# Optimization experiments

Hardware: AMD Instinct MI355X
Metric: run time of the kernel (lower is better)

Reference implementation:

```python
import jax, jax.numpy as jnp
import numpy as np
import math

HID = 128
NH = 8
HD = HID // NH
NL = 3
CLIP = 10.0
EPS = 1e-5

def _ln(x, g, b):
    mu = jnp.mean(x, axis=-1, keepdims=True)
    var = jnp.var(x, axis=-1, keepdims=True)
    return (x - mu) * jax.lax.rsqrt(var + EPS) * g + b

def _layer(h, e_bias1, e_gate2, g1, b1, wh, g2, b2, w1, w2):
    B, N, _ = h.shape
    h_in = h
    hn = _ln(h, g1, b1)
    qkv = hn @ wh                                   # (B,N,3H)
    q, k, v = jnp.split(qkv, 3, axis=-1)
    q = q.reshape(B, N, NH, HD).transpose(0, 2, 1, 3)  # (B,nh,N,hd)
    k = k.reshape(B, N, NH, HD).transpose(0, 2, 1, 3)
    v = v.reshape(B, N, NH, HD).transpose(0, 2, 1, 3)
    att = jnp.einsum('bhid,bhjd->bhij', q, k) * (1.0 / math.sqrt(HD))
    att = jax.nn.softmax(att + e_bias1, axis=-1) * e_gate2
    y = jnp.einsum('bhij,bhjd->bhid', att, v)
    y = y.transpose(0, 2, 1, 3).reshape(B, N, HID)
    z = _ln(y + h_in, g2, b2)
    mlp = jax.nn.relu(z @ w1) @ w2
    return mlp + y

def setup_inputs() -> dict:
    key = jax.random.key(0)
    ks = jax.random.split(key, 9)
    d = {
        'node_features': jax.random.normal(ks[0], (16, 256, 2), jnp.float32),
        'edge_features': jax.random.normal(ks[1], (16, 256, 256, 1), jnp.float32),
        'Wn': jax.random.normal(ks[2], (2, HID), jnp.float32) * 0.5,
        'We_in': jax.random.normal(ks[3], (1, HID), jnp.float32) * 0.1,
        'ln1_g': jnp.ones((NL, HID), jnp.float32),
        'ln1_b': jnp.zeros((NL, HID), jnp.float32),
        'Wh': jax.random.normal(ks[4], (NL, HID, 3 * HID), jnp.float32) * (1.0 / math.sqrt(HID)),
        'We': jax.random.normal(ks[5], (NL, HID, 2 * NH), jnp.float32) * (1.0 / math.sqrt(HID)),
        'ln2_g': jnp.ones((NL, HID), jnp.float32),
        'ln2_b': jnp.zeros((NL, HID), jnp.float32),
        'W1': jax.random.normal(ks[6], (NL, HID, 4 * HID), jnp.float32) * (1.0 / math.sqrt(HID)),
        'W2': jax.random.normal(ks[7], (NL, 4 * HID, HID), jnp.float32) * (1.0 / math.sqrt(4 * HID)),
        'Wdec': jax.random.normal(ks[8], (HID, 1), jnp.float32) * (1.0 / math.sqrt(HID)),
    }
    return d

def reference(node_features, edge_features, Wn, We_in, ln1_g, ln1_b, Wh, We, ln2_g, ln2_b, W1, W2, Wdec):
    h = node_features @ Wn                              # (B,N,H)
    e = edge_features @ We_in                           # (B,N,N,H)
    for i in range(NL):
        ee = e @ We[i]                                  # (B,N,N,2*nh)
        ee = ee.transpose(0, 3, 1, 2)                   # (B,2*nh,N,N)
        e1, e2 = ee[:, :NH], ee[:, NH:]
        h = _layer(h, e1, e2, ln1_g[i], ln1_b[i], Wh[i], ln2_g[i], ln2_b[i], W1[i], W2[i])
    out = h @ Wdec                                      # (B,N,1)
    out = CLIP * jnp.tanh(out / math.sqrt(HID))
    return out
```

## Files before the change

kernel.cpp:

```cpp
#include <hip/hip_runtime.h>
#include <math.h>

#define HID 128
#define NHEAD 8
#define NL 3
#define NS 256
#define ROWS 4096

typedef __attribute__((ext_vector_type(8))) short bf16x8;
typedef __attribute__((ext_vector_type(4))) float f32x4;

__device__ __forceinline__ float us2f(unsigned short s) { return __uint_as_float(((unsigned)s) << 16); }
__device__ __forceinline__ unsigned short f2b(float f) {
    unsigned u = __float_as_uint(f);
    return (unsigned short)((u + 0x7fff + ((u >> 16) & 1)) >> 16);
}

__global__ __launch_bounds__(256) void k_prep(
    const float* __restrict__ Wh, const float* __restrict__ W1, const float* __restrict__ W2,
    const float* __restrict__ We_in, const float* __restrict__ We,
    const float* __restrict__ nf, const float* __restrict__ Wn,
    unsigned short* __restrict__ WhH, unsigned short* __restrict__ WhL,
    unsigned short* __restrict__ W1H, unsigned short* __restrict__ W1L,
    unsigned short* __restrict__ W2H, unsigned short* __restrict__ W2L,
    float* __restrict__ sbuf, float* __restrict__ h)
{
    int b = blockIdx.x, t = threadIdx.x;
    if (b >= 529) {
        int idx = (b - 529) * 256 + t;
        int r = idx >> 7, c = idx & 127;
        h[idx] = nf[2 * r] * Wn[c] + nf[2 * r + 1] * Wn[HID + c];
        return;
    }
    if (b == 528) {
        if (t < NL * 2 * NHEAD) {
            int l = t / (2 * NHEAD), j = t % (2 * NHEAD);
            float acc = 0.f;
            for (int c = 0; c < HID; ++c)
                acc += We_in[c] * We[(long)(l * HID + c) * (2 * NHEAD) + j];
            sbuf[t] = acc;
        }
        return;
    }
    const float* S; unsigned short *OH, *OL; int K, N, kt, nt;
    if (b < 144) {
        int l = b / 48, rem = b % 48; kt = rem & 3; nt = rem >> 2; K = 128; N = 384;
        S = Wh + (long)l * 128 * 384; OH = WhH + (long)l * 384 * 128; OL = WhL + (long)l * 384 * 128;
    } else if (b < 336) {
        int b2 = b - 144; int l = b2 / 64, rem = b2 % 64; kt = rem & 3; nt = rem >> 2; K = 128; N = 512;
        S = W1 + (long)l * 128 * 512; OH = W1H + (long)l * 512 * 128; OL = W1L + (long)l * 512 * 128;
    } else {
        int b2 = b - 336; int l = b2 / 64, rem = b2 % 64; kt = rem & 15; nt = rem >> 4; K = 512; N = 128;
        S = W2 + (long)l * 512 * 128; OH = W2H + (long)l * 128 * 512; OL = W2L + (long)l * 128 * 512;
    }
    __shared__ float sm[32][33];
    int i0 = t >> 5, j = t & 31;
#pragma unroll
    for (int p = 0; p < 4; ++p) {
        int i = i0 + p * 8;
        sm[i][j] = S[(long)(kt * 32 + i) * N + nt * 32 + j];
    }
    __syncthreads();
#pragma unroll
    for (int p = 0; p < 4; ++p) {
        int n = i0 + p * 8;
        float v = sm[j][n];
        unsigned short hh = f2b(v);
        long o = (long)(nt * 32 + n) * K + kt * 32 + j;
        OH[o] = hh; OL[o] = f2b(v - us2f(hh));
    }
}

__global__ __launch_bounds__(256) void k_fgemm(
    const float* __restrict__ x, const float* __restrict__ x2,
    const float* __restrict__ g, const float* __restrict__ b,
    const unsigned short* __restrict__ WH, const unsigned short* __restrict__ WL,
    float* __restrict__ Cf, unsigned short* __restrict__ Ch, unsigned short* __restrict__ Cl,
    int Nc, int mode)
{
    __shared__ unsigned short sAh[64 * 136], sAl[64 * 136];
    __shared__ unsigned short sWh[64 * 136], sWl[64 * 136];
    int t = threadIdx.x;
    int row0 = blockIdx.y * 64, col0 = blockIdx.x * 64;

#pragma unroll
    for (int p = 0; p < 4; ++p) {
        int rr = (t >> 4) + p * 16, ck = t & 15;
        *(uint4*)&sWh[rr * 136 + ck * 8] = *(const uint4*)&WH[(long)(col0 + rr) * 128 + ck * 8];
        *(uint4*)&sWl[rr * 136 + ck * 8] = *(const uint4*)&WL[(long)(col0 + rr) * 128 + ck * 8];
    }
#pragma unroll
    for (int pass = 0; pass < 2; ++pass) {
        int row = pass * 32 + (t >> 3);
        int p = t & 7, cb = p * 16;
        float v[16];
        const float* xp = x + (long)(row0 + row) * HID + cb;
#pragma unroll
        for (int j = 0; j < 16; j += 4) *(float4*)&v[j] = *(const float4*)(xp + j);
        if (x2) {
            const float* yp = x2 + (long)(row0 + row) * HID + cb;
#pragma unroll
            for (int j = 0; j < 16; j += 4) {
                float4 r4 = *(const float4*)(yp + j);
                v[j] += r4.x; v[j+1] += r4.y; v[j+2] += r4.z; v[j+3] += r4.w;
            }
        }
        float s = 0.f, s2 = 0.f;
#pragma unroll
        for (int j = 0; j < 16; ++j) { s += v[j]; s2 += v[j] * v[j]; }
        s  += __shfl_xor(s, 1);  s  += __shfl_xor(s, 2);  s  += __shfl_xor(s, 4);
        s2 += __shfl_xor(s2, 1); s2 += __shfl_xor(s2, 2); s2 += __shfl_xor(s2, 4);
        float mu  = s * (1.f / HID);
        float var = s2 * (1.f / HID) - mu * mu;
        float inv = rsqrtf(var + 1e-5f);
        unsigned short hi[16], lo[16];
#pragma unroll
        for (int j = 0; j < 16; ++j) {
            int c = cb + j;
            float o = (v[j] - mu) * inv * g[c] + b[c];
            hi[j] = f2b(o); lo[j] = f2b(o - us2f(hi[j]));
        }
        *(uint4*)&sAh[row * 136 + cb]     = *(uint4*)&hi[0];
        *(uint4*)&sAh[row * 136 + cb + 8] = *(uint4*)&hi[8];
        *(uint4*)&sAl[row * 136 + cb]     = *(uint4*)&lo[0];
        *(uint4*)&sAl[row * 136 + cb + 8] = *(uint4*)&lo[8];
    }
    __syncthreads();

    int w = t >> 6, lane = t & 63;
    int m = lane & 15, quad = lane >> 4;
    f32x4 acc[4];
#pragma unroll
    for (int i = 0; i < 4; ++i) acc[i] = (f32x4){0.f, 0.f, 0.f, 0.f};
#pragma unroll
    for (int c = 0; c < 4; ++c) {
        bf16x8 ah = *(const bf16x8*)&sAh[(w * 16 + m) * 136 + c * 32 + quad * 8];
        bf16x8 al = *(const bf16x8*)&sAl[(w * 16 + m) * 136 + c * 32 + quad * 8];
#pragma unroll
        for (int nt = 0; nt < 4; ++nt) {
            bf16x8 wh = *(const bf16x8*)&sWh[(nt * 16 + m) * 136 + c * 32 + quad * 8];
            bf16x8 wl = *(const bf16x8*)&sWl[(nt * 16 + m) * 136 + c * 32 + quad * 8];
            acc[nt] = __builtin_amdgcn_mfma_f32_16x16x32_bf16(ah, wh, acc[nt], 0, 0, 0);
            acc[nt] = __builtin_amdgcn_mfma_f32_16x16x32_bf16(ah, wl, acc[nt], 0, 0, 0);
            acc[nt] = __builtin_amdgcn_mfma_f32_16x16x32_bf16(al, wh, acc[nt], 0, 0, 0);
        }
    }
#pragma unroll
    for (int nt = 0; nt < 4; ++nt) {
#pragma unroll
        for (int r = 0; r < 4; ++r) {
            int row = row0 + w * 16 + quad * 4 + r;
            int col = col0 + nt * 16 + m;
            float v = acc[nt][r];
            if (mode == 0) {
                Cf[(long)row * Nc + col] = v;
            } else {
                v = fmaxf(v, 0.f);
                unsigned short hh = f2b(v);
                Ch[(long)row * Nc + col] = hh;
                Cl[(long)row * Nc + col] = f2b(v - us2f(hh));
            }
        }
    }
}

__global__ __launch_bounds__(256, 3) void k_w2ln(
    const unsigned short* __restrict__ Ah, const unsigned short* __restrict__ Al,
    const unsigned short* __restrict__ WH, const unsigned short* __restrict__ WL,
    const float* __restrict__ yres, float* __restrict__ hout,
    const float* __restrict__ Wdec, float* __restrict__ out)
{
    __shared__ unsigned short sA[2][16 * 72];
    __shared__ unsigned short sW[2][128 * 72];
    int t = threadIdx.x;
    int row0 = blockIdx.x * 16;
    int w = t >> 6, lane = t & 63;
    int m = lane & 15, quad = lane >> 4;
    f32x4 acc[2];
    acc[0] = (f32x4){0.f,0.f,0.f,0.f}; acc[1] = (f32x4){0.f,0.f,0.f,0.f};

    for (int ks = 0; ks < 512; ks += 64) {
        if (ks) __syncthreads();
        {
            int pl = t >> 7, tt = t & 127;
            int r = tt >> 3, ck = tt & 7;
            const unsigned short* src = pl ? Al : Ah;
            *(uint4*)&sA[pl][r * 72 + ck * 8] = *(const uint4*)&src[(long)(row0 + r) * 512 + ks + ck * 8];
        }
        {
            int r0 = t >> 3, ck = t & 7;
#pragma unroll
            for (int p = 0; p < 4; ++p) {
                int n = r0 + p * 32;
                *(uint4*)&sW[0][n * 72 + ck * 8] = *(const uint4*)&WH[(long)n * 512 + ks + ck * 8];
                *(uint4*)&sW[1][n * 72 + ck * 8] = *(const uint4*)&WL[(long)n * 512 + ks + ck * 8];
            }
        }
        __syncthreads();
#pragma unroll
        for (int c = 0; c < 2; ++c) {
            bf16x8 ah = *(const bf16x8*)&sA[0][m * 72 + c * 32 + quad * 8];
            bf16x8 al = *(const bf16x8*)&sA[1][m * 72 + c * 32 + quad * 8];
#pragma unroll
            for (int nt = 0; nt < 2; ++nt) {
                int n = w * 32 + nt * 16 + m;
                bf16x8 wh = *(const bf16x8*)&sW[0][n * 72 + c * 32 + quad * 8];
                bf16x8 wl = *(const bf16x8*)&sW[1][n * 72 + c * 32 + quad * 8];
                acc[nt] = __builtin_amdgcn_mfma_f32_16x16x32_bf16(ah, wh, acc[nt], 0, 0, 0);
                acc[nt] = __builtin_amdgcn_mfma_f32_16x16x32_bf16(ah, wl, acc[nt], 0, 0, 0);
                acc[nt] = __builtin_amdgcn_mfma_f32_16x16x32_bf16(al, wh, acc[nt], 0, 0, 0);
            }
        }
    }
    __syncthreads();
    float* ht = (float*)&sW[0][0];
#pragma unroll
    for (int nt = 0; nt < 2; ++nt) {
#pragma unroll
        for (int r = 0; r < 4; ++r) {
            int row = quad * 4 + r;
            int col = w * 32 + nt * 16 + m;
            float v = acc[nt][r] + yres[(long)(row0 + row) * HID + col];
            hout[(long)(row0 + row) * HID + col] = v;
            ht[row * 132 + col] = v;
        }
    }
    __syncthreads();
    if (Wdec) {
        int row = t >> 4, sub = t & 15;
        float v[8];
        *(float4*)&v[0] = *(const float4*)&ht[row * 132 + sub * 8];
        *(float4*)&v[4] = *(const float4*)&ht[row * 132 + sub * 8 + 4];
        float a = 0.f;
#pragma unroll
        for (int j = 0; j < 8; ++j) a += v[j] * Wdec[sub * 8 + j];
        a += __shfl_xor(a, 1); a += __shfl_xor(a, 2); a += __shfl_xor(a, 4); a += __shfl_xor(a, 8);
        if (sub == 0) out[row0 + row] = 10.f * tanhf(a * 0.08838834764831845f);
    }
}

#define PAS (NS + 8)
__global__ __launch_bounds__(256) void k_attn(const float* __restrict__ qkv,
                                              const float* __restrict__ ef,
                                              const float* __restrict__ sbuf,
                                              int layer,
                                              float* __restrict__ y) {
    __shared__ float Ks[NS][20];
    __shared__ unsigned short Vh[16][PAS];
    __shared__ unsigned short Vl[16][PAS];
    __shared__ unsigned short Pa[4][16][PAS];
    int bid = blockIdx.x;
    int q4 = bid & 3, hh = (bid >> 2) & 7, bb = bid >> 5;
    int t = threadIdx.x;
    {
        const float* kr = qkv + ((long)(bb * NS + t)) * 384 + HID + hh * 16;
        *(float4*)&Ks[t][0]  = *(const float4*)kr;
        *(float4*)&Ks[t][4]  = *(const float4*)(kr + 4);
        *(float4*)&Ks[t][8]  = *(const float4*)(kr + 8);
        *(float4*)&Ks[t][12] = *(const float4*)(kr + 12);
        const float* vr = kr + HID;
        float vv[16];
        *(float4*)&vv[0]  = *(const float4*)vr;
        *(float4*)&vv[4]  = *(const float4*)(vr + 4);
        *(float4*)&vv[8]  = *(const float4*)(vr + 8);
        *(float4*)&vv[12] = *(const float4*)(vr + 12);
#pragma unroll
        for (int d = 0; d < 16; ++d) {
            unsigned short hi = f2b(vv[d]);
            Vh[d][t] = hi;
            Vl[d][t] = f2b(vv[d] - us2f(hi));
        }
    }
    __syncthreads();
    int w = t >> 6, lane = t & 63;
    float s1  = sbuf[layer * 16 + hh];
    float s2g = sbuf[layer * 16 + NHEAD + hh];
    int m = lane & 15, quad = lane >> 4;
    unsigned short* Paw = &Pa[w][0][0];
    for (int it = 0; it < 4; ++it) {
        int r0 = q4 * 64 + w * 16 + it * 4;
        float q[4][16];
#pragma unroll
        for (int rr = 0; rr < 4; ++rr) {
            const float* qr = qkv + ((long)(bb * NS + r0 + rr)) * 384 + hh * 16;
            *(float4*)&q[rr][0]  = *(const float4*)qr;
            *(float4*)&q[rr][4]  = *(const float4*)(qr + 4);
            *(float4*)&q[rr][8]  = *(const float4*)(qr + 8);
            *(float4*)&q[rr][12] = *(const float4*)(qr + 12);
        }
        float sc[4][4];
#pragma unroll
        for (int i = 0; i < 4; ++i) {
            int c = i * 64 + lane;
            float kk[16];
            *(float4*)&kk[0]  = *(const float4*)&Ks[c][0];
            *(float4*)&kk[4]  = *(const float4*)&Ks[c][4];
            *(float4*)&kk[8]  = *(const float4*)&Ks[c][8];
            *(float4*)&kk[12] = *(const float4*)&Ks[c][12];
#pragma unroll
            for (int rr = 0; rr < 4; ++rr) {
                float d0 = 0.f;
#pragma unroll
                for (int d = 0; d < 16; ++d) d0 += q[rr][d] * kk[d];
                sc[rr][i] = d0;
            }
        }
#pragma unroll
        for (int rr = 0; rr < 4; ++rr) {
            long eb = ((long)(bb * NS + r0 + rr)) * NS;
            float e0 = ef[eb + lane],       e1 = ef[eb + 64 + lane];
            float e2 = ef[eb + 128 + lane], e3 = ef[eb + 192 + lane];
            float x0 = sc[rr][0] * 0.25f + e0 * s1;
            float x1 = sc[rr][1] * 0.25f + e1 * s1;
            float x2 = sc[rr][2] * 0.25f + e2 * s1;
            float x3 = sc[rr][3] * 0.25f + e3 * s1;
            float mm = fmaxf(fmaxf(x0, x1), fmaxf(x2, x3));
#pragma unroll
            for (int o = 32; o; o >>= 1) mm = fmaxf(mm, __shfl_xor(mm, o));
            float p0 = __expf(x0 - mm), p1 = __expf(x1 - mm);
            float p2 = __expf(x2 - mm), p3 = __expf(x3 - mm);
            float sum = p0 + p1 + p2 + p3;
#pragma unroll
            for (int o = 32; o; o >>= 1) sum += __shfl_xor(sum, o);
            float inv = s2g / sum;
            int prow = it * 4 + rr;
            Paw[prow * PAS + lane]       = f2b(p0 * inv * e0);
            Paw[prow * PAS + 64 + lane]  = f2b(p1 * inv * e1);
            Paw[prow * PAS + 128 + lane] = f2b(p2 * inv * e2);
            Paw[prow * PAS + 192 + lane] = f2b(p3 * inv * e3);
        }
    }
    f32x4 acc = (f32x4){0.f, 0.f, 0.f, 0.f};
#pragma unroll
    for (int s = 0; s < 8; ++s) {
        bf16x8 pf = *(const bf16x8*)&Paw[m * PAS + s * 32 + quad * 8];
        bf16x8 vh = *(const bf16x8*)&Vh[m][s * 32 + quad * 8];
        bf16x8 vl = *(const bf16x8*)&Vl[m][s * 32 + quad * 8];
        acc = __builtin_amdgcn_mfma_f32_16x16x32_bf16(pf, vh, acc, 0, 0, 0);
        acc = __builtin_amdgcn_mfma_f32_16x16x32_bf16(pf, vl, acc, 0, 0, 0);
    }
#pragma unroll
    for (int r = 0; r < 4; ++r) {
        int row = q4 * 64 + w * 16 + quad * 4 + r;
        y[((long)(bb * NS + row)) * HID + hh * 16 + m] = acc[r];
    }
}

extern "C" void kernel_launch(void* const* d_in, const int* in_sizes, int n_in,
                              void* d_out, int out_size, void* d_ws, size_t ws_size,
                              hipStream_t stream) {
    const float* nf    = (const float*)d_in[0];
    const float* ef    = (const float*)d_in[1];
    const float* Wn    = (const float*)d_in[2];
    const float* We_in = (const float*)d_in[3];
    const float* ln1g  = (const float*)d_in[4];
    const float* ln1b  = (const float*)d_in[5];
    const float* Wh    = (const float*)d_in[6];
    const float* We    = (const float*)d_in[7];
    const float* ln2g  = (const float*)d_in[8];
    const float* ln2b  = (const float*)d_in[9];
    const float* W1    = (const float*)d_in[10];
    const float* W2    = (const float*)d_in[11];
    const float* Wdec  = (const float*)d_in[12];

    float* ws   = (float*)d_ws;
    float* sbuf = ws;
    float* h    = ws + 64;
    float* y    = h + ROWS * HID;
    float* qkv  = y + ROWS * HID;
    unsigned short* hidH = (unsigned short*)(qkv + (long)ROWS * 384);
    unsigned short* hidL = hidH + (long)ROWS * 512;
    unsigned short* WhH  = hidL + (long)ROWS * 512;
    unsigned short* WhL  = WhH + (long)NL * 384 * 128;
    unsigned short* W1H  = WhL + (long)NL * 384 * 128;
    unsigned short* W1L  = W1H + (long)NL * 512 * 128;
    unsigned short* W2H  = W1L + (long)NL * 512 * 128;
    unsigned short* W2L  = W2H + (long)NL * 128 * 512;

    k_prep<<<529 + ROWS * HID / 256, 256, 0, stream>>>(Wh, W1, W2, We_in, We, nf, Wn,
                                    WhH, WhL, W1H, W1L, W2H, W2L, sbuf, h);
    for (int l = 0; l < NL; ++l) {
        k_fgemm<<<dim3(6, 64), 256, 0, stream>>>(h, nullptr,
            ln1g + l * HID, ln1b + l * HID,
            WhH + (long)l * 384 * 128, WhL + (long)l * 384 * 128,
            qkv, nullptr, nullptr, 384, 0);
        k_attn<<<512, 256, 0, stream>>>(qkv, ef, sbuf, l, y);
        k_fgemm<<<dim3(8, 64), 256, 0, stream>>>(y, h,
            ln2g + l * HID, ln2b + l * HID,
            W1H + (long)l * 512 * 128, W1L + (long)l * 512 * 128,
            nullptr, hidH, hidL, 512, 1);
        int last = (l == NL - 1);
        k_w2ln<<<ROWS / 16, 256, 0, stream>>>(hidH, hidL,
            W2H + (long)l * 128 * 512, W2L + (long)l * 128 * 512,
            y, h, last ? Wdec : nullptr, (float*)d_out);
    }
}
```

Baseline: 231.6 us.

## Fuse input embedding into first GEMM, split W2 by columns, drop softmax max

The node embedding moves out of the prep kernel and into the first LN+QKV GEMM, which also writes h. The W2 GEMM is split into two 64-column tiles to double the block count, and the decoder becomes its own small kernel. In fgemm the weight loads are issued into registers before the LayerNorm work so their latency overlaps it. Attention softmax drops the max subtraction, which saves a reduction but risks exp overflow for large logits. A barrier is also added before the P·V MMA.

```diff
diff --git a/kernel.cpp b/kernel.cpp
--- a/kernel.cpp
+++ b/kernel.cpp
@@ -19,19 +19,12 @@
 __global__ __launch_bounds__(256) void k_prep(
     const float* __restrict__ Wh, const float* __restrict__ W1, const float* __restrict__ W2,
     const float* __restrict__ We_in, const float* __restrict__ We,
-    const float* __restrict__ nf, const float* __restrict__ Wn,
     unsigned short* __restrict__ WhH, unsigned short* __restrict__ WhL,
     unsigned short* __restrict__ W1H, unsigned short* __restrict__ W1L,
     unsigned short* __restrict__ W2H, unsigned short* __restrict__ W2L,
-    float* __restrict__ sbuf, float* __restrict__ h)
+    float* __restrict__ sbuf)
 {
     int b = blockIdx.x, t = threadIdx.x;
-    if (b >= 529) {
-        int idx = (b - 529) * 256 + t;
-        int r = idx >> 7, c = idx & 127;
-        h[idx] = nf[2 * r] * Wn[c] + nf[2 * r + 1] * Wn[HID + c];
-        return;
-    }
     if (b == 528) {
         if (t < NL * 2 * NHEAD) {
             int l = t / (2 * NHEAD), j = t % (2 * NHEAD);
@@ -73,6 +66,7 @@
 
 __global__ __launch_bounds__(256) void k_fgemm(
     const float* __restrict__ x, const float* __restrict__ x2,
+    const float* __restrict__ nf, const float* __restrict__ Wn, float* __restrict__ hout,
     const float* __restrict__ g, const float* __restrict__ b,
     const unsigned short* __restrict__ WH, const unsigned short* __restrict__ WL,
     float* __restrict__ Cf, unsigned short* __restrict__ Ch, unsigned short* __restrict__ Cl,
@@ -83,26 +77,40 @@
     int t = threadIdx.x;
     int row0 = blockIdx.y * 64, col0 = blockIdx.x * 64;
 
-#pragma unroll
-    for (int p = 0; p < 4; ++p) {
-        int rr = (t >> 4) + p * 16, ck = t & 15;
-        *(uint4*)&sWh[rr * 136 + ck * 8] = *(const uint4*)&WH[(long)(col0 + rr) * 128 + ck * 8];
-        *(uint4*)&sWl[rr * 136 + ck * 8] = *(const uint4*)&WL[(long)(col0 + rr) * 128 + ck * 8];
+    uint4 wreg[8];
+    {
+        int rr0 = t >> 4, ck = t & 15;
+#pragma unroll
+        for (int p = 0; p < 4; ++p) {
+            wreg[p]     = *(const uint4*)&WH[(long)(col0 + rr0 + p * 16) * 128 + ck * 8];
+            wreg[4 + p] = *(const uint4*)&WL[(long)(col0 + rr0 + p * 16) * 128 + ck * 8];
+        }
     }
 #pragma unroll
     for (int pass = 0; pass < 2; ++pass) {
         int row = pass * 32 + (t >> 3);
         int p = t & 7, cb = p * 16;
         float v[16];
-        const float* xp = x + (long)(row0 + row) * HID + cb;
-#pragma unroll
-        for (int j = 0; j < 16; j += 4) *(float4*)&v[j] = *(const float4*)(xp + j);
-        if (x2) {
-            const float* yp = x2 + (long)(row0 + row) * HID + cb;
-#pragma unroll
-            for (int j = 0; j < 16; j += 4) {
-                float4 r4 = *(const float4*)(yp + j);
-                v[j] += r4.x; v[j+1] += r4.y; v[j+2] += r4.z; v[j+3] += r4.w;
+        if (nf) {
+            float n0 = nf[2 * (row0 + row)], n1 = nf[2 * (row0 + row) + 1];
+#pragma unroll
+            for (int j = 0; j < 16; ++j) v[j] = n0 * Wn[cb + j] + n1 * Wn[HID + cb + j];
+            if (blockIdx.x == 0) {
+#pragma unroll
+                for (int j = 0; j < 16; j += 4)
+                    *(float4*)&hout[(long)(row0 + row) * HID + cb + j] = *(float4*)&v[j];
+            }
+        } else {
+            const float* xp = x + (long)(row0 + row) * HID + cb;
+#pragma unroll
+            for (int j = 0; j < 16; j += 4) *(float4*)&v[j] = *(const float4*)(xp + j);
+            if (x2) {
+                const float* yp = x2 + (long)(row0 + row) * HID + cb;
+#pragma unroll
+                for (int j = 0; j < 16; j += 4) {
+                    float4 r4 = *(const float4*)(yp + j);
+                    v[j] += r4.x; v[j+1] += r4.y; v[j+2] += r4.z; v[j+3] += r4.w;
+                }
             }
         }
         float s = 0.f, s2 = 0.f;
@@ -124,6 +132,14 @@
         *(uint4*)&sAh[row * 136 + cb + 8] = *(uint4*)&hi[8];
         *(uint4*)&sAl[row * 136 + cb]     = *(uint4*)&lo[0];
         *(uint4*)&sAl[row * 136 + cb + 8] = *(uint4*)&lo[8];
+    }
+    {
+        int rr0 = t >> 4, ck = t & 15;
+#pragma unroll
+        for (int p = 0; p < 4; ++p) {
+            *(uint4*)&sWh[(rr0 + p * 16) * 136 + ck * 8] = wreg[p];
+            *(uint4*)&sWl[(rr0 + p * 16) * 136 + ck * 8] = wreg[4 + p];
+        }
     }
     __syncthreads();
 
@@ -164,20 +180,18 @@
     }
 }
 
-__global__ __launch_bounds__(256, 3) void k_w2ln(
+__global__ __launch_bounds__(256, 4) void k_w2(
     const unsigned short* __restrict__ Ah, const unsigned short* __restrict__ Al,
     const unsigned short* __restrict__ WH, const unsigned short* __restrict__ WL,
-    const float* __restrict__ yres, float* __restrict__ hout,
-    const float* __restrict__ Wdec, float* __restrict__ out)
+    const float* __restrict__ yres, float* __restrict__ hout)
 {
     __shared__ unsigned short sA[2][16 * 72];
-    __shared__ unsigned short sW[2][128 * 72];
+    __shared__ unsigned short sW[2][64 * 72];
     int t = threadIdx.x;
-    int row0 = blockIdx.x * 16;
+    int ct = blockIdx.x, row0 = blockIdx.y * 16, col0 = ct * 64;
     int w = t >> 6, lane = t & 63;
     int m = lane & 15, quad = lane >> 4;
-    f32x4 acc[2];
-    acc[0] = (f32x4){0.f,0.f,0.f,0.f}; acc[1] = (f32x4){0.f,0.f,0.f,0.f};
+    f32x4 acc = (f32x4){0.f, 0.f, 0.f, 0.f};
 
     for (int ks = 0; ks < 512; ks += 64) {
         if (ks) __syncthreads();
@@ -188,54 +202,29 @@
             *(uint4*)&sA[pl][r * 72 + ck * 8] = *(const uint4*)&src[(long)(row0 + r) * 512 + ks + ck * 8];
         }
         {
-            int r0 = t >> 3, ck = t & 7;
-#pragma unroll
-            for (int p = 0; p < 4; ++p) {
-                int n = r0 + p * 32;
-                *(uint4*)&sW[0][n * 72 + ck * 8] = *(const uint4*)&WH[(long)n * 512 + ks + ck * 8];
-                *(uint4*)&sW[1][n * 72 + ck * 8] = *(const uint4*)&WL[(long)n * 512 + ks + ck * 8];
-            }
+            int n = t >> 2, c2 = (t & 3) * 2;
+            *(uint4*)&sW[0][n * 72 + c2 * 8]       = *(const uint4*)&WH[(long)(col0 + n) * 512 + ks + c2 * 8];
+            *(uint4*)&sW[0][n * 72 + (c2 + 1) * 8] = *(const uint4*)&WH[(long)(col0 + n) * 512 + ks + (c2 + 1) * 8];
+            *(uint4*)&sW[1][n * 72 + c2 * 8]       = *(const uint4*)&WL[(long)(col0 + n) * 512 + ks + c2 * 8];
+            *(uint4*)&sW[1][n * 72 + (c2 + 1) * 8] = *(const uint4*)&WL[(long)(col0 + n) * 512 + ks + (c2 + 1) * 8];
         }
         __syncthreads();
 #pragma unroll
         for (int c = 0; c < 2; ++c) {
             bf16x8 ah = *(const bf16x8*)&sA[0][m * 72 + c * 32 + quad * 8];
             bf16x8 al = *(const bf16x8*)&sA[1][m * 72 + c * 32 + quad * 8];
-#pragma unroll
-            for (int nt = 0; nt < 2; ++nt) {
-                int n = w * 32 + nt * 16 + m;
-                bf16x8 wh = *(const bf16x8*)&sW[0][n * 72 + c * 32 + quad * 8];
-                bf16x8 wl = *(const bf16x8*)&sW[1][n * 72 + c * 32 + quad * 8];
-                acc[nt] = __builtin_amdgcn_mfma_f32_16x16x32_bf16(ah, wh, acc[nt], 0, 0, 0);
-                acc[nt] = __builtin_amdgcn_mfma_f32_16x16x32_bf16(ah, wl, acc[nt], 0, 0, 0);
-                acc[nt] = __builtin_amdgcn_mfma_f32_16x16x32_bf16(al, wh, acc[nt], 0, 0, 0);
-            }
-        }
-    }
-    __syncthreads();
-    float* ht = (float*)&sW[0][0];
-#pragma unroll
-    for (int nt = 0; nt < 2; ++nt) {
-#pragma unroll
-        for (int r = 0; r < 4; ++r) {
-            int row = quad * 4 + r;
-            int col = w * 32 + nt * 16 + m;
-            float v = acc[nt][r] + yres[(long)(row0 + row) * HID + col];
-            hout[(long)(row0 + row) * HID + col] = v;
-            ht[row * 132 + col] = v;
-        }
-    }
-    __syncthreads();
-    if (Wdec) {
-        int row = t >> 4, sub = t & 15;
-        float v[8];
-        *(float4*)&v[0] = *(const float4*)&ht[row * 132 + sub * 8];
-        *(float4*)&v[4] = *(const float4*)&ht[row * 132 + sub * 8 + 4];
-        float a = 0.f;
-#pragma unroll
-        for (int j = 0; j < 8; ++j) a += v[j] * Wdec[sub * 8 + j];
-        a += __shfl_xor(a, 1); a += __shfl_xor(a, 2); a += __shfl_xor(a, 4); a += __shfl_xor(a, 8);
-        if (sub == 0) out[row0 + row] = 10.f * tanhf(a * 0.08838834764831845f);
+            bf16x8 wh = *(const bf16x8*)&sW[0][(w * 16 + m) * 72 + c * 32 + quad * 8];
+            bf16x8 wl = *(const bf16x8*)&sW[1][(w * 16 + m) * 72 + c * 32 + quad * 8];
+            acc = __builtin_amdgcn_mfma_f32_16x16x32_bf16(ah, wh, acc, 0, 0, 0);
+            acc = __builtin_amdgcn_mfma_f32_16x16x32_bf16(ah, wl, acc, 0, 0, 0);
+            acc = __builtin_amdgcn_mfma_f32_16x16x32_bf16(al, wh, acc, 0, 0, 0);
+        }
+    }
+#pragma unroll
+    for (int r = 0; r < 4; ++r) {
+        int row = row0 + quad * 4 + r;
+        int col = col0 + w * 16 + m;
+        hout[(long)row * HID + col] = acc[r] + yres[(long)row * HID + col];
     }
 }
 
@@ -310,15 +299,10 @@
             long eb = ((long)(bb * NS + r0 + rr)) * NS;
             float e0 = ef[eb + lane],       e1 = ef[eb + 64 + lane];
             float e2 = ef[eb + 128 + lane], e3 = ef[eb + 192 + lane];
-            float x0 = sc[rr][0] * 0.25f + e0 * s1;
-            float x1 = sc[rr][1] * 0.25f + e1 * s1;
-            float x2 = sc[rr][2] * 0.25f + e2 * s1;
-            float x3 = sc[rr][3] * 0.25f + e3 * s1;
-            float mm = fmaxf(fmaxf(x0, x1), fmaxf(x2, x3));
-#pragma unroll
-            for (int o = 32; o; o >>= 1) mm = fmaxf(mm, __shfl_xor(mm, o));
-            float p0 = __expf(x0 - mm), p1 = __expf(x1 - mm);
-            float p2 = __expf(x2 - mm), p3 = __expf(x3 - mm);
+            float p0 = __expf(sc[rr][0] * 0.25f + e0 * s1);
+            float p1 = __expf(sc[rr][1] * 0.25f + e1 * s1);
+            float p2 = __expf(sc[rr][2] * 0.25f + e2 * s1);
+            float p3 = __expf(sc[rr][3] * 0.25f + e3 * s1);
             float sum = p0 + p1 + p2 + p3;
 #pragma unroll
             for (int o = 32; o; o >>= 1) sum += __shfl_xor(sum, o);
@@ -330,6 +314,7 @@
             Paw[prow * PAS + 192 + lane] = f2b(p3 * inv * e3);
         }
     }
+    __syncthreads();
     f32x4 acc = (f32x4){0.f, 0.f, 0.f, 0.f};
 #pragma unroll
     for (int s = 0; s < 8; ++s) {
@@ -344,6 +329,18 @@
         int row = q4 * 64 + w * 16 + quad * 4 + r;
         y[((long)(bb * NS + row)) * HID + hh * 16 + m] = acc[r];
     }
+}
+
+__global__ __launch_bounds__(256) void k_dec(const float* __restrict__ h,
+                                             const float* __restrict__ Wdec,
+                                             float* __restrict__ out) {
+    int w = threadIdx.x >> 6, lane = threadIdx.x & 63;
+    int row = blockIdx.x * 4 + w;
+    float a = h[(long)row * HID + lane] * Wdec[lane]
+            + h[(long)row * HID + 64 + lane] * Wdec[64 + lane];
+#pragma unroll
+    for (int o = 32; o; o >>= 1) a += __shfl_xor(a, o);
+    if (lane == 0) out[row] = 10.f * tanhf(a * 0.08838834764831845f);
 }
 
 extern "C" void kernel_launch(void* const* d_in, const int* in_sizes, int n_in,
@@ -377,21 +374,22 @@
     unsigned short* W2H  = W1L + (long)NL * 512 * 128;
     unsigned short* W2L  = W2H + (long)NL * 128 * 512;
 
-    k_prep<<<529 + ROWS * HID / 256, 256, 0, stream>>>(Wh, W1, W2, We_in, We, nf, Wn,
-                                    WhH, WhL, W1H, W1L, W2H, W2L, sbuf, h);
+    k_prep<<<529, 256, 0, stream>>>(Wh, W1, W2, We_in, We,
+                                    WhH, WhL, W1H, W1L, W2H, W2L, sbuf);
     for (int l = 0; l < NL; ++l) {
         k_fgemm<<<dim3(6, 64), 256, 0, stream>>>(h, nullptr,
+            (l == 0) ? nf : nullptr, Wn, h,
             ln1g + l * HID, ln1b + l * HID,
             WhH + (long)l * 384 * 128, WhL + (long)l * 384 * 128,
             qkv, nullptr, nullptr, 384, 0);
         k_attn<<<512, 256, 0, stream>>>(qkv, ef, sbuf, l, y);
         k_fgemm<<<dim3(8, 64), 256, 0, stream>>>(y, h,
+            nullptr, Wn, nullptr,
             ln2g + l * HID, ln2b + l * HID,
             W1H + (long)l * 512 * 128, W1L + (long)l * 512 * 128,
             nullptr, hidH, hidL, 512, 1);
-        int last = (l == NL - 1);
-        k_w2ln<<<ROWS / 16, 256, 0, stream>>>(hidH, hidL,
-            W2H + (long)l * 128 * 512, W2L + (long)l * 128 * 512,
-            y, h, last ? Wdec : nullptr, (float*)d_out);
-    }
-}
+        k_w2<<<dim3(2, 256), 256, 0, stream>>>(hidH, hidL,
+            W2H + (long)l * 128 * 512, W2L + (long)l * 128 * 512, y, h);
+    }
+    k_dec<<<ROWS / 4, 256, 0, stream>>>(h, Wdec, (float*)d_out);
+}
```

New measurement: 250.4 us. +8.1%, slower.
